# Kernel tuning notes

Hardware: AMD Instinct MI355X
Metric: run time of the kernel (lower is better)

## Reference

```python
import jax, jax.numpy as jnp
import numpy as np

H = 16  # num heads
DH = 64  # head dim


def setup_inputs() -> dict:
    key = jax.random.key(0)
    ks = jax.random.split(key, 9)
    d = 1024
    s = 0.02
    return {
        "hidden_states": jax.random.normal(ks[0], (16, 1024, d), jnp.float32),
        "Wq": jax.random.normal(ks[1], (d, d), jnp.float32) * s,
        "bq": jax.random.normal(ks[2], (d,), jnp.float32) * s,
        "Wk": jax.random.normal(ks[3], (d, d), jnp.float32) * s,
        "bk": jax.random.normal(ks[4], (d,), jnp.float32) * s,
        "Wv": jax.random.normal(ks[5], (d, d), jnp.float32) * s,
        "bv": jax.random.normal(ks[6], (d,), jnp.float32) * s,
        "Wo": jax.random.normal(ks[7], (d, d), jnp.float32) * s,
        "bo": jax.random.normal(ks[8], (d,), jnp.float32) * s,
    }


def _heads(x):
    b, s, _ = x.shape
    return x.reshape(b, s, H, DH).transpose(0, 2, 1, 3)  # [B,H,S,Dh]


def reference(hidden_states, Wq, bq, Wk, bk, Wv, bv, Wo, bo):
    # torch nn.Linear: y = x @ W.T + b; weights here are [out, in]
    q = _heads(hidden_states @ Wq.T + bq)
    k = _heads(hidden_states @ Wk.T + bk)
    v = _heads(hidden_states @ Wv.T + bv)
    scores = jnp.einsum("bhqd,bhkd->bhqk", q, k) / jnp.sqrt(jnp.float32(DH))
    probs = jax.nn.softmax(scores, axis=-1)
    ctx = jnp.einsum("bhqk,bhkd->bhqd", probs, v)
    b, _, s, _ = ctx.shape
    ctx = ctx.transpose(0, 2, 1, 3).reshape(b, s, H * DH)
    out = ctx @ Wo.T + bo
    # module returns (attention_output, weights=None); return array only
    return out
```

## Files before the change

kernel.cpp:

```cpp
#include <hip/hip_runtime.h>
#include <hip/hip_bf16.h>
#include <stdint.h>


typedef short bf16x8 __attribute__((ext_vector_type(8)));
typedef float f32x4 __attribute__((ext_vector_type(4)));
typedef float f32x16 __attribute__((ext_vector_type(16)));
typedef unsigned short ushort_t;
typedef ushort_t us8 __attribute__((ext_vector_type(8)));

__device__ __forceinline__ ushort_t f2b(float f) {
    unsigned x;
    __builtin_memcpy(&x, &f, 4);
    unsigned r = (x + 0x7fffu + ((x >> 16) & 1u)) >> 16;
    return (ushort_t)r;
}

__device__ __forceinline__ void glds16(const void* g, void* l) {
    __builtin_amdgcn_global_load_lds(
        (const __attribute__((address_space(1))) void*)g,
        (__attribute__((address_space(3))) void*)l, 16, 0, 0);
}

#define MFMA16(a, b, c) __builtin_amdgcn_mfma_f32_16x16x32_bf16((a), (b), (c), 0, 0, 0)
#define MFMA32(a, b, c) __builtin_amdgcn_mfma_f32_32x32x16_bf16((a), (b), (c), 0, 0, 0)

__global__ __launch_bounds__(256, 8) void cvt4_kernel(
    const float* __restrict__ s0, const float* __restrict__ s1,
    const float* __restrict__ s2, const float* __restrict__ s3,
    ushort_t* __restrict__ d0, ushort_t* __restrict__ d1,
    ushort_t* __restrict__ d2, ushort_t* __restrict__ d3, int n8)
{
    const float* in = (blockIdx.y == 0) ? s0 : (blockIdx.y == 1) ? s1
                       : (blockIdx.y == 2) ? s2 : s3;
    ushort_t* out = (blockIdx.y == 0) ? d0 : (blockIdx.y == 1) ? d1
                       : (blockIdx.y == 2) ? d2 : d3;
    int i = blockIdx.x * 256 + threadIdx.x;
    if (i >= n8) return;
    const float4* p = (const float4*)in + (size_t)i * 2;
    float4 a = p[0], b = p[1];
    us8 v;
    v[0] = f2b(a.x); v[1] = f2b(a.y); v[2] = f2b(a.z); v[3] = f2b(a.w);
    v[4] = f2b(b.x); v[5] = f2b(b.y); v[6] = f2b(b.z); v[7] = f2b(b.w);
    *((us8*)out + i) = v;
}

__global__ __launch_bounds__(256, 8) void cvt1_kernel(
    const float* __restrict__ in, ushort_t* __restrict__ out, int n8)
{
    int i = blockIdx.x * 256 + threadIdx.x;
    if (i >= n8) return;
    const float4* p = (const float4*)in + (size_t)i * 2;
    float4 a = p[0], b = p[1];
    us8 v;
    v[0] = f2b(a.x); v[1] = f2b(a.y); v[2] = f2b(a.z); v[3] = f2b(a.w);
    v[4] = f2b(b.x); v[5] = f2b(b.y); v[6] = f2b(b.z); v[7] = f2b(b.w);
    *((us8*)out + i) = v;
}

template <bool OUTF>
__global__ __launch_bounds__(256, 2) void gemm_bias_kernel(
    const ushort_t* __restrict__ A,
    const ushort_t* __restrict__ W0, const ushort_t* __restrict__ W1, const ushort_t* __restrict__ W2,
    const float* __restrict__ b0, const float* __restrict__ b1, const float* __restrict__ b2,
    void* __restrict__ C0, void* __restrict__ C1, void* __restrict__ C2,
    float s0, float s1, float s2,
    int M, int N, int K)
{
    const ushort_t* W = (blockIdx.z == 0) ? W0 : ((blockIdx.z == 1) ? W1 : W2);
    const float* bias = (blockIdx.z == 0) ? b0 : ((blockIdx.z == 1) ? b1 : b2);
    void* C = (blockIdx.z == 0) ? C0 : ((blockIdx.z == 1) ? C1 : C2);
    const float scale = (blockIdx.z == 0) ? s0 : ((blockIdx.z == 1) ? s1 : s2);

    __shared__ ushort_t As[128 * 64];
    __shared__ ushort_t Bs[128 * 64];

    const int tid = threadIdx.x;
    const int lane = tid & 63;
    const int wave = tid >> 6;
    const int bm = blockIdx.x * 128;
    const int bn = blockIdx.y * 128;
    const int wm = (wave >> 1) * 64;
    const int wn = (wave & 1) * 64;
    const int r32 = lane & 31;
    const int g = lane >> 5;

    f32x16 acc[2][2] = {};

    for (int k0 = 0; k0 < K; k0 += 64) {
        __syncthreads();
#pragma unroll
        for (int it = 0; it < 4; ++it) {
            int cid = it * 256 + tid;
            int r = cid >> 3;
            int s = cid & 7;
            int sc = s ^ (r & 7);
            glds16(A + (size_t)(bm + r) * K + k0 + sc * 8, As + cid * 8);
            glds16(W + (size_t)(bn + r) * K + k0 + sc * 8, Bs + cid * 8);
        }
        __syncthreads();
#pragma unroll
        for (int kk = 0; kk < 4; ++kk) {
            bf16x8 af[2], bfr[2];
#pragma unroll
            for (int i = 0; i < 2; ++i) {
                int row = wm + i * 32 + r32;
                int ch = (kk * 2 + g) ^ (row & 7);
                af[i] = *(const bf16x8*)(As + row * 64 + ch * 8);
                int rowb = wn + i * 32 + r32;
                int chb = (kk * 2 + g) ^ (rowb & 7);
                bfr[i] = *(const bf16x8*)(Bs + rowb * 64 + chb * 8);
            }
#pragma unroll
            for (int i = 0; i < 2; ++i)
#pragma unroll
                for (int j = 0; j < 2; ++j)
                    acc[i][j] = MFMA32(af[i], bfr[j], acc[i][j]);
        }
    }

#pragma unroll
    for (int j = 0; j < 2; ++j) {
        int col = bn + wn + j * 32 + r32;
        float bv = bias[col];
#pragma unroll
        for (int i = 0; i < 2; ++i) {
            int rbase = bm + wm + i * 32 + 4 * g;
#pragma unroll
            for (int reg = 0; reg < 16; ++reg) {
                int row = rbase + (reg & 3) + 8 * (reg >> 2);
                float v = (acc[i][j][reg] + bv) * scale;
                if (OUTF)
                    ((float*)C)[(size_t)row * N + col] = v;
                else
                    ((ushort_t*)C)[(size_t)row * N + col] = f2b(v);
            }
        }
    }
}

__global__ __launch_bounds__(256, 4) void transpose_v_kernel(
    const ushort_t* __restrict__ V, ushort_t* __restrict__ Vt)
{
    __shared__ ushort_t t[64 * 65];
    const int bh = blockIdx.x;
    const int st = blockIdx.y;
    const int b = bh >> 4, h = bh & 15;
    const int tid = threadIdx.x;

#pragma unroll
    for (int i = 0; i < 16; ++i) {
        int e = i * 256 + tid;
        int s = e >> 6, d = e & 63;
        t[s * 65 + d] = V[(size_t)(b * 1024 + st * 64 + s) * 1024 + h * 64 + d];
    }
    __syncthreads();
#pragma unroll
    for (int i = 0; i < 16; ++i) {
        int e = i * 256 + tid;
        int d = e >> 6, s = e & 63;
        Vt[(size_t)(bh * 64 + d) * 1024 + st * 64 + s] = t[s * 65 + d];
    }
}

__global__ __launch_bounds__(256, 2) void attn_kernel(
    const ushort_t* __restrict__ Q, const ushort_t* __restrict__ K,
    const ushort_t* __restrict__ Vt, ushort_t* __restrict__ ctx)
{
    __shared__ ushort_t Ks[2][64 * 64];
    __shared__ ushort_t Vs[2][64 * 64];
    __shared__ ushort_t Ps[4][32 * 72];

    const int bh = blockIdx.x;
    const int qt = blockIdx.y;
    const int b = bh >> 4, h = bh & 15;
    const int tid = threadIdx.x;
    const int lane = tid & 63;
    const int wave = tid >> 6;
    const int q = lane >> 4;
    const int ml = lane & 15;

    const int cid0 = tid;
    const int cid1 = 256 + tid;
    const int r0 = cid0 >> 3, sc0 = (cid0 & 7) ^ (r0 & 7);
    const int r1 = cid1 >> 3, sc1 = (cid1 & 7) ^ (r1 & 7);
    const ushort_t* Kbase = K + (size_t)(b * 1024) * 1024 + h * 64;
    const ushort_t* Vbase = Vt + (size_t)(bh * 64) * 1024;

    bf16x8 qf[2][2];
#pragma unroll
    for (int mg = 0; mg < 2; ++mg) {
        int row = b * 1024 + qt * 128 + wave * 32 + mg * 16 + ml;
        const ushort_t* qp = Q + (size_t)row * 1024 + h * 64;
        qf[mg][0] = *(const bf16x8*)(qp + q * 8);
        qf[mg][1] = *(const bf16x8*)(qp + 32 + q * 8);
    }

    bf16x8 ones;
#pragma unroll
    for (int i = 0; i < 8; ++i) ones[i] = (short)0x3F80;

    f32x4 o[2][4] = {};
    f32x4 ls[2] = {};
    ushort_t* Pw = Ps[wave];

    glds16(Kbase + (size_t)r0 * 1024 + sc0 * 8, Ks[0] + cid0 * 8);
    glds16(Vbase + (size_t)r0 * 1024 + sc0 * 8, Vs[0] + cid0 * 8);
    glds16(Kbase + (size_t)r1 * 1024 + sc1 * 8, Ks[0] + cid1 * 8);
    glds16(Vbase + (size_t)r1 * 1024 + sc1 * 8, Vs[0] + cid1 * 8);

    for (int kt = 0; kt < 16; ++kt) {
        const int cur = kt & 1, nxt = cur ^ 1;
        __syncthreads();
        if (kt + 1 < 16) {
            const ushort_t* Kn = Kbase + (size_t)(kt + 1) * 64 * 1024;
            const ushort_t* Vn = Vbase + (kt + 1) * 64;
            glds16(Kn + (size_t)r0 * 1024 + sc0 * 8, Ks[nxt] + cid0 * 8);
            glds16(Vn + (size_t)r0 * 1024 + sc0 * 8, Vs[nxt] + cid0 * 8);
            glds16(Kn + (size_t)r1 * 1024 + sc1 * 8, Ks[nxt] + cid1 * 8);
            glds16(Vn + (size_t)r1 * 1024 + sc1 * 8, Vs[nxt] + cid1 * 8);
        }
        const ushort_t* Kc = Ks[cur];
        const ushort_t* Vc = Vs[cur];

#pragma unroll
        for (int n = 0; n < 4; ++n) {
            int row = n * 16 + ml;
            int c0 = q ^ (row & 7);
            int c1 = (4 + q) ^ (row & 7);
            bf16x8 k0 = *(const bf16x8*)(Kc + row * 64 + c0 * 8);
            bf16x8 k1 = *(const bf16x8*)(Kc + row * 64 + c1 * 8);
#pragma unroll
            for (int mg = 0; mg < 2; ++mg) {
                f32x4 z = {};
                z = MFMA16(k0, qf[mg][0], z);
                z = MFMA16(k1, qf[mg][1], z);
                float p0 = __builtin_amdgcn_exp2f(z[0]);
                float p1 = __builtin_amdgcn_exp2f(z[1]);
                float p2 = __builtin_amdgcn_exp2f(z[2]);
                float p3 = __builtin_amdgcn_exp2f(z[3]);
                __hip_bfloat162 h01 = __float22bfloat162_rn(make_float2(p0, p1));
                __hip_bfloat162 h23 = __float22bfloat162_rn(make_float2(p2, p3));
                uint2 dd;
                __builtin_memcpy(&dd.x, &h01, 4);
                __builtin_memcpy(&dd.y, &h23, 4);
                *(uint2*)(Pw + (mg * 16 + ml) * 72 + n * 16 + q * 4) = dd;
            }
        }

#pragma unroll
        for (int mg = 0; mg < 2; ++mg) {
            bf16x8 pf0 = *(const bf16x8*)(Pw + (mg * 16 + ml) * 72 + q * 8);
            bf16x8 pf1 = *(const bf16x8*)(Pw + (mg * 16 + ml) * 72 + 32 + q * 8);
            ls[mg] = MFMA16(pf0, ones, ls[mg]);
            ls[mg] = MFMA16(pf1, ones, ls[mg]);
#pragma unroll
            for (int n = 0; n < 4; ++n) {
                int row = n * 16 + ml;
                int c0 = q ^ (row & 7);
                int c1 = (4 + q) ^ (row & 7);
                bf16x8 v0 = *(const bf16x8*)(Vc + row * 64 + c0 * 8);
                bf16x8 v1 = *(const bf16x8*)(Vc + row * 64 + c1 * 8);
                o[mg][n] = MFMA16(pf0, v0, o[mg][n]);
                o[mg][n] = MFMA16(pf1, v1, o[mg][n]);
            }
        }
    }

    const int orow_base = b * 1024 + qt * 128 + wave * 32;
#pragma unroll
    for (int mg = 0; mg < 2; ++mg) {
#pragma unroll
        for (int r = 0; r < 4; ++r) {
            float lv = 1.0f / ls[mg][r];
            int orow = orow_base + mg * 16 + q * 4 + r;
#pragma unroll
            for (int n = 0; n < 4; ++n) {
                ctx[(size_t)orow * 1024 + h * 64 + n * 16 + ml] =
                    f2b(o[mg][n][r] * lv);
            }
        }
    }
}

extern "C" void kernel_launch(void* const* d_in, const int* in_sizes, int n_in,
                              void* d_out, int out_size, void* d_ws, size_t ws_size,
                              hipStream_t stream)
{
    const float* X  = (const float*)d_in[0];
    const float* Wq = (const float*)d_in[1];
    const float* bq = (const float*)d_in[2];
    const float* Wk = (const float*)d_in[3];
    const float* bk = (const float*)d_in[4];
    const float* Wv = (const float*)d_in[5];
    const float* bv = (const float*)d_in[6];
    const float* Wo = (const float*)d_in[7];
    const float* bo = (const float*)d_in[8];

    const int D = 1024;
    const int M = in_sizes[0] / D;
    const int Bb = M / 1024;
    const size_t MD = (size_t)M * D;
    const size_t DD = (size_t)D * D;

    ushort_t* ws  = (ushort_t*)d_ws;
    ushort_t* Xbf = ws;
    ushort_t* Qb  = ws + MD;
    ushort_t* Kb  = ws + 2 * MD;
    ushort_t* Vb  = ws + 3 * MD;
    ushort_t* Wqb = ws + 4 * MD;
    ushort_t* Wkb = Wqb + DD;
    ushort_t* Wvb = Wkb + DD;
    ushort_t* Wob = Wvb + DD;
    ushort_t* Vtb = Xbf;
    ushort_t* ctx = Vb;

    dim3 blk(256);

    cvt1_kernel<<<(int)(MD / 8 / 256), blk, 0, stream>>>(X, Xbf, (int)(MD / 8));
    cvt4_kernel<<<dim3((int)(DD / 8 / 256), 4), blk, 0, stream>>>(
        Wq, Wk, Wv, Wo, Wqb, Wkb, Wvb, Wob, (int)(DD / 8));

    const float qscale = 1.4426950408889634f * 0.125f;
    dim3 gqkv(M / 128, D / 128, 3);
    gemm_bias_kernel<false><<<gqkv, blk, 0, stream>>>(Xbf, Wqb, Wkb, Wvb, bq, bk, bv,
                                                      Qb, Kb, Vb,
                                                      qscale, 1.0f, 1.0f, M, D, D);

    transpose_v_kernel<<<dim3(Bb * 16, 16), blk, 0, stream>>>(Vb, Vtb);

    attn_kernel<<<dim3(Bb * 16, 8), blk, 0, stream>>>(Qb, Kb, Vtb, ctx);

    dim3 go(M / 128, D / 128, 1);
    gemm_bias_kernel<true><<<go, blk, 0, stream>>>(ctx, Wob, Wob, Wob, bo, bo, bo,
                                                   d_out, d_out, d_out,
                                                   1.0f, 1.0f, 1.0f, M, D, D);
}
```

Before: 395.1 us.

## Replace GEMM with 256x256 tiled, double-buffered 8-wave pipelined kernel

Replaces the 128x128 single-buffered GEMM with a 256x256-tile kernel using 512 threads, 16x16x32 MFMAs, and double-buffered LDS stages loaded asynchronously with explicit vmcnt waits and barriers interleaving loads with compute. It adds block-index swizzling for L2 locality and raises MFMA wave priority during compute. The aim is to hide global-load latency and raise arithmetic intensity per tile. The loop structure hardcodes K=1024 (16 k-steps) and grid swizzle assumes tile counts divisible by 8, and the larger tiles give fewer blocks per GPU.

```diff
diff --git a/kernel.cpp b/kernel.cpp
--- a/kernel.cpp
+++ b/kernel.cpp
@@ -5,7 +5,6 @@
 
 typedef short bf16x8 __attribute__((ext_vector_type(8)));
 typedef float f32x4 __attribute__((ext_vector_type(4)));
-typedef float f32x16 __attribute__((ext_vector_type(16)));
 typedef unsigned short ushort_t;
 typedef ushort_t us8 __attribute__((ext_vector_type(8)));
 
@@ -23,7 +22,6 @@
 }
 
 #define MFMA16(a, b, c) __builtin_amdgcn_mfma_f32_16x16x32_bf16((a), (b), (c), 0, 0, 0)
-#define MFMA32(a, b, c) __builtin_amdgcn_mfma_f32_32x32x16_bf16((a), (b), (c), 0, 0, 0)
 
 __global__ __launch_bounds__(256, 8) void cvt4_kernel(
     const float* __restrict__ s0, const float* __restrict__ s1,
@@ -59,84 +57,154 @@
 }
 
 template <bool OUTF>
-__global__ __launch_bounds__(256, 2) void gemm_bias_kernel(
+__global__ __launch_bounds__(512) void gemm256_kernel(
     const ushort_t* __restrict__ A,
     const ushort_t* __restrict__ W0, const ushort_t* __restrict__ W1, const ushort_t* __restrict__ W2,
     const float* __restrict__ b0, const float* __restrict__ b1, const float* __restrict__ b2,
     void* __restrict__ C0, void* __restrict__ C1, void* __restrict__ C2,
-    float s0, float s1, float s2,
-    int M, int N, int K)
+    float s0, float s1, float s2, int N, int K)
 {
     const ushort_t* W = (blockIdx.z == 0) ? W0 : ((blockIdx.z == 1) ? W1 : W2);
     const float* bias = (blockIdx.z == 0) ? b0 : ((blockIdx.z == 1) ? b1 : b2);
     void* C = (blockIdx.z == 0) ? C0 : ((blockIdx.z == 1) ? C1 : C2);
     const float scale = (blockIdx.z == 0) ? s0 : ((blockIdx.z == 1) ? s1 : s2);
 
-    __shared__ ushort_t As[128 * 64];
-    __shared__ ushort_t Bs[128 * 64];
+    __shared__ ushort_t lds[2][4][256 * 32];
 
     const int tid = threadIdx.x;
     const int lane = tid & 63;
     const int wave = tid >> 6;
-    const int bm = blockIdx.x * 128;
-    const int bn = blockIdx.y * 128;
-    const int wm = (wave >> 1) * 64;
-    const int wn = (wave & 1) * 64;
-    const int r32 = lane & 31;
-    const int g = lane >> 5;
-
-    f32x16 acc[2][2] = {};
-
-    for (int k0 = 0; k0 < K; k0 += 64) {
-        __syncthreads();
-#pragma unroll
-        for (int it = 0; it < 4; ++it) {
-            int cid = it * 256 + tid;
-            int r = cid >> 3;
-            int s = cid & 7;
-            int sc = s ^ (r & 7);
-            glds16(A + (size_t)(bm + r) * K + k0 + sc * 8, As + cid * 8);
-            glds16(W + (size_t)(bn + r) * K + k0 + sc * 8, Bs + cid * 8);
-        }
-        __syncthreads();
-#pragma unroll
-        for (int kk = 0; kk < 4; ++kk) {
-            bf16x8 af[2], bfr[2];
-#pragma unroll
-            for (int i = 0; i < 2; ++i) {
-                int row = wm + i * 32 + r32;
-                int ch = (kk * 2 + g) ^ (row & 7);
-                af[i] = *(const bf16x8*)(As + row * 64 + ch * 8);
-                int rowb = wn + i * 32 + r32;
-                int chb = (kk * 2 + g) ^ (rowb & 7);
-                bfr[i] = *(const bf16x8*)(Bs + rowb * 64 + chb * 8);
-            }
-#pragma unroll
-            for (int i = 0; i < 2; ++i)
-#pragma unroll
-                for (int j = 0; j < 2; ++j)
-                    acc[i][j] = MFMA32(af[i], bfr[j], acc[i][j]);
-        }
-    }
-
-#pragma unroll
-    for (int j = 0; j < 2; ++j) {
-        int col = bn + wn + j * 32 + r32;
-        float bv = bias[col];
-#pragma unroll
-        for (int i = 0; i < 2; ++i) {
-            int rbase = bm + wm + i * 32 + 4 * g;
-#pragma unroll
-            for (int reg = 0; reg < 16; ++reg) {
-                int row = rbase + (reg & 3) + 8 * (reg >> 2);
-                float v = (acc[i][j][reg] + bv) * scale;
+    const int wr = wave >> 2;
+    const int wc = wave & 3;
+    const int rl = lane & 15;
+    const int ck = lane >> 4;
+
+    const int gx = gridDim.x;
+    const int flat = blockIdx.y * gx + blockIdx.x;
+    const int cpx = (gx * gridDim.y) >> 3;
+    const int swz = (flat & 7) * cpx + (flat >> 3);
+    const int bm = (swz % gx) * 256;
+    const int bn = (swz / gx) * 256;
+
+    const ushort_t* Ag = A + (size_t)bm * K;
+    const ushort_t* Bg = W + (size_t)bn * K;
+
+    const int q0 = tid, q1 = 512 + tid;
+    const int sr0 = q0 >> 2, sc0 = (q0 & 3) * 8;
+    const int sr1 = q1 >> 2, sc1 = (q1 & 3) * 8;
+
+#define STG(gbase, kcol, dst) do { \
+    glds16((gbase) + (size_t)sr0 * K + (kcol) + sc0, (dst) + q0 * 8); \
+    glds16((gbase) + (size_t)sr1 * K + (kcol) + sc1, (dst) + q1 * 8); } while (0)
+
+#define BARRIER() do { \
+    __builtin_amdgcn_sched_barrier(0); \
+    asm volatile("s_barrier" ::: "memory"); \
+    __builtin_amdgcn_sched_barrier(0); } while (0)
+
+#define VMCNT(n) asm volatile("s_waitcnt vmcnt(" #n ")" ::: "memory")
+
+    f32x4 acc[8][4] = {};
+    bf16x8 af[8], bfr[2];
+
+    const int aoff = (wr * 128 + rl) * 32 + ck * 8;
+    const int boff = (wc * 64 + rl) * 32 + ck * 8;
+
+#define LDA(buf, kh) do { _Pragma("unroll") \
+    for (int mi = 0; mi < 8; ++mi) \
+        af[mi] = *(const bf16x8*)(&lds[buf][kh][0] + aoff + mi * 512); } while (0)
+#define LDB(buf, kh, nb) do { \
+    bfr[0] = *(const bf16x8*)(&lds[buf][2 + (kh)][0] + boff + (nb) * 1024); \
+    bfr[1] = *(const bf16x8*)(&lds[buf][2 + (kh)][0] + boff + (nb) * 1024 + 512); } while (0)
+#define MM(nb) do { __builtin_amdgcn_s_setprio(1); _Pragma("unroll") \
+    for (int mi = 0; mi < 8; ++mi) { \
+        acc[mi][2*(nb)]   = MFMA16(af[mi], bfr[0], acc[mi][2*(nb)]); \
+        acc[mi][2*(nb)+1] = MFMA16(af[mi], bfr[1], acc[mi][2*(nb)+1]); } \
+    __builtin_amdgcn_s_setprio(0); } while (0)
+
+    STG(Ag, 0,  &lds[0][0][0]);
+    STG(Bg, 0,  &lds[0][2][0]);
+    STG(Ag, 32, &lds[0][1][0]);
+    STG(Bg, 32, &lds[0][3][0]);
+    STG(Ag, 64, &lds[1][0][0]);
+    STG(Bg, 64, &lds[1][2][0]);
+    VMCNT(4);
+    BARRIER();
+
+#pragma unroll 1
+    for (int i = 0; i < 7; ++i) {
+        const int t = 2 * i;
+        const int kc1 = (t + 1) * 64, kc2 = (t + 2) * 64, kc3 = (t + 3) * 64;
+        LDA(0, 0); LDB(0, 0, 0);
+        STG(Ag, kc1 + 32, &lds[1][1][0]);
+        BARRIER(); MM(0); BARRIER();
+        LDB(0, 0, 1);
+        STG(Bg, kc1 + 32, &lds[1][3][0]);
+        BARRIER(); MM(1); BARRIER();
+        LDA(0, 1); LDB(0, 1, 0);
+        STG(Ag, kc2, &lds[0][0][0]);
+        BARRIER(); MM(0); BARRIER();
+        LDB(0, 1, 1);
+        STG(Bg, kc2, &lds[0][2][0]);
+        VMCNT(4);
+        BARRIER(); MM(1); BARRIER();
+        LDA(1, 0); LDB(1, 0, 0);
+        STG(Ag, kc2 + 32, &lds[0][1][0]);
+        BARRIER(); MM(0); BARRIER();
+        LDB(1, 0, 1);
+        STG(Bg, kc2 + 32, &lds[0][3][0]);
+        BARRIER(); MM(1); BARRIER();
+        LDA(1, 1); LDB(1, 1, 0);
+        STG(Ag, kc3, &lds[1][0][0]);
+        BARRIER(); MM(0); BARRIER();
+        LDB(1, 1, 1);
+        STG(Bg, kc3, &lds[1][2][0]);
+        VMCNT(4);
+        BARRIER(); MM(1); BARRIER();
+    }
+
+    {
+        const int kc15 = 15 * 64;
+        LDA(0, 0); LDB(0, 0, 0);
+        STG(Ag, kc15 + 32, &lds[1][1][0]);
+        BARRIER(); MM(0); BARRIER();
+        LDB(0, 0, 1);
+        STG(Bg, kc15 + 32, &lds[1][3][0]);
+        BARRIER(); MM(1); BARRIER();
+        LDA(0, 1); LDB(0, 1, 0);
+        BARRIER(); MM(0); BARRIER();
+        LDB(0, 1, 1);
+        VMCNT(0);
+        BARRIER(); MM(1); BARRIER();
+        LDA(1, 0); LDB(1, 0, 0); MM(0);
+        LDB(1, 0, 1); MM(1);
+        LDA(1, 1); LDB(1, 1, 0); MM(0);
+        LDB(1, 1, 1); MM(1);
+    }
+
+#pragma unroll
+    for (int ni = 0; ni < 4; ++ni) {
+        const int col = bn + wc * 64 + ni * 16 + rl;
+        const float bv = bias[col];
+#pragma unroll
+        for (int mi = 0; mi < 8; ++mi) {
+            const int rbase = bm + wr * 128 + mi * 16 + ck * 4;
+#pragma unroll
+            for (int r = 0; r < 4; ++r) {
+                float v = (acc[mi][ni][r] + bv) * scale;
                 if (OUTF)
-                    ((float*)C)[(size_t)row * N + col] = v;
+                    ((float*)C)[(size_t)(rbase + r) * N + col] = v;
                 else
-                    ((ushort_t*)C)[(size_t)row * N + col] = f2b(v);
+                    ((ushort_t*)C)[(size_t)(rbase + r) * N + col] = f2b(v);
             }
         }
     }
+#undef STG
+#undef BARRIER
+#undef VMCNT
+#undef LDA
+#undef LDB
+#undef MM
 }
 
 __global__ __launch_bounds__(256, 4) void transpose_v_kernel(
@@ -316,23 +384,26 @@
     ushort_t* ctx = Vb;
 
     dim3 blk(256);
+    dim3 blk512(512);
 
     cvt1_kernel<<<(int)(MD / 8 / 256), blk, 0, stream>>>(X, Xbf, (int)(MD / 8));
     cvt4_kernel<<<dim3((int)(DD / 8 / 256), 4), blk, 0, stream>>>(
         Wq, Wk, Wv, Wo, Wqb, Wkb, Wvb, Wob, (int)(DD / 8));
 
     const float qscale = 1.4426950408889634f * 0.125f;
-    dim3 gqkv(M / 128, D / 128, 3);
-    gemm_bias_kernel<false><<<gqkv, blk, 0, stream>>>(Xbf, Wqb, Wkb, Wvb, bq, bk, bv,
-                                                      Qb, Kb, Vb,
-                                                      qscale, 1.0f, 1.0f, M, D, D);
+    dim3 gqkv(M / 256, D / 256, 3);
+    gemm256_kernel<false><<<gqkv, blk512, 0, stream>>>(Xbf, Wqb, Wkb, Wvb,
+                                                       bq, bk, bv,
+                                                       Qb, Kb, Vb,
+                                                       qscale, 1.0f, 1.0f, D, D);
 
     transpose_v_kernel<<<dim3(Bb * 16, 16), blk, 0, stream>>>(Vb, Vtb);
 
     attn_kernel<<<dim3(Bb * 16, 8), blk, 0, stream>>>(Qb, Kb, Vtb, ctx);
 
-    dim3 go(M / 128, D / 128, 1);
-    gemm_bias_kernel<true><<<go, blk, 0, stream>>>(ctx, Wob, Wob, Wob, bo, bo, bo,
-                                                   d_out, d_out, d_out,
-                                                   1.0f, 1.0f, 1.0f, M, D, D);
-}
+    dim3 go(M / 256, D / 256, 1);
+    gemm256_kernel<true><<<go, blk512, 0, stream>>>(ctx, Wob, Wob, Wob,
+                                                    bo, bo, bo,
+                                                    d_out, d_out, d_out,
+                                                    1.0f, 1.0f, 1.0f, D, D);
+}
```

After: 412.1 us. 1.04x slower.
